# Performance work log

Measured on AMD Instinct MI355X. Metric: run time of the kernel, lower is better.

## Reference

```python
import jax, jax.numpy as jnp
import numpy as np

N, E, D = 50000, 800000, 128
NODE_IN, EDGE_IN, STEPS = 19, 4, 5
EPS = 1e-5

def leaky(x):
    return jnp.where(x > 0, x, 0.05 * x)

def mlp3(x, W1, b1, W2, b2, W3, b3):
    x = leaky(x @ W1 + b1)
    x = leaky(x @ W2 + b2)
    return x @ W3 + b3

def layer_norm(x, g, b):
    m = jnp.mean(x, axis=-1, keepdims=True)
    v = jnp.var(x, axis=-1, keepdims=True)
    return (x - m) * jax.lax.rsqrt(v + EPS) * g + b

def batch_norm(x, g, b):
    # training-mode BatchNorm1d: biased batch stats over node dim
    m = jnp.mean(x, axis=0)
    v = jnp.var(x, axis=0)
    return (x - m) * jax.lax.rsqrt(v + EPS) * g + b

def gcn_conv(x, src, dst, W, b):
    # PyG GCNConv: add self loops, sym-normalize by deg^{-1/2}, aggregate at dst
    h = x @ W  # [N, D]
    deg = jax.ops.segment_sum(jnp.ones(E, x.dtype), dst, num_segments=N) + 1.0
    dis = jax.lax.rsqrt(deg)
    msg = h[src] * (dis[src] * dis[dst])[:, None]  # [E, D]
    agg = jax.ops.segment_sum(msg, dst, num_segments=N) + h * (dis * dis)[:, None]
    return agg + b


def setup_inputs() -> dict:
    key = jax.random.key(0)
    ks = iter(jax.random.split(key, 64))
    w = lambda shape: jax.random.normal(next(ks), shape, jnp.float32) * 0.05
    z = lambda: jnp.zeros((D,), jnp.float32)
    o = lambda: jnp.ones((D,), jnp.float32)
    inp = {
        'node_feat': jax.random.normal(next(ks), (N, NODE_IN), jnp.float32),
        'edge_feat': jax.random.normal(next(ks), (E, EDGE_IN), jnp.float32),
        'edge_index': jax.random.randint(next(ks), (2, E), 0, N, jnp.int32),
        'enc_node_W1': w((NODE_IN, D)), 'enc_node_b1': z(),
        'enc_node_W2': w((D, D)), 'enc_node_b2': z(),
        'enc_node_W3': w((D, D)), 'enc_node_b3': z(),
        'enc_node_ln_g': o(), 'enc_node_ln_b': z(),
        'enc_edge_W1': w((EDGE_IN, D)), 'enc_edge_b1': z(),
        'enc_edge_W2': w((D, D)), 'enc_edge_b2': z(),
        'enc_edge_W3': w((D, D)), 'enc_edge_b3': z(),
        'enc_edge_ln_g': o(), 'enc_edge_ln_b': z(),
        'proc_W': w((STEPS, 2, D, D)),
        'proc_b': jnp.zeros((STEPS, 2, D), jnp.float32),
        'proc_bn_g': jnp.ones((STEPS, D), jnp.float32),
        'proc_bn_b': jnp.zeros((STEPS, D), jnp.float32),
        'dec_W1': w((D, D)), 'dec_b1': z(),
        'dec_W2': w((D, D)), 'dec_b2': z(),
        'dec_W3': w((D, D)), 'dec_b3': z(),
        'dec_ln_g': o(), 'dec_ln_b': z(),
    }
    return inp


def reference(node_feat, edge_feat, edge_index,
              enc_node_W1, enc_node_b1, enc_node_W2, enc_node_b2, enc_node_W3, enc_node_b3,
              enc_node_ln_g, enc_node_ln_b,
              enc_edge_W1, enc_edge_b1, enc_edge_W2, enc_edge_b2, enc_edge_W3, enc_edge_b3,
              enc_edge_ln_g, enc_edge_ln_b,
              proc_W, proc_b, proc_bn_g, proc_bn_b,
              dec_W1, dec_b1, dec_W2, dec_b2, dec_W3, dec_b3, dec_ln_g, dec_ln_b):
    src, dst = edge_index[0], edge_index[1]
    # encode
    hn = layer_norm(mlp3(node_feat, enc_node_W1, enc_node_b1, enc_node_W2, enc_node_b2,
                         enc_node_W3, enc_node_b3), enc_node_ln_g, enc_node_ln_b)
    he = layer_norm(mlp3(edge_feat, enc_edge_W1, enc_edge_b1, enc_edge_W2, enc_edge_b2,
                         enc_edge_W3, enc_edge_b3), enc_edge_ln_g, enc_edge_ln_b)
    # scatter-mean edge features onto source nodes
    cnt = jax.ops.segment_sum(jnp.ones(E, hn.dtype), src, num_segments=N)
    hn = hn + jax.ops.segment_sum(he, src, num_segments=N) / jnp.maximum(cnt, 1.0)[:, None]
    # 5 residual GCN processor steps (GCNConv -> LeakyReLU -> BN -> GCNConv)
    for s in range(STEPS):
        x = gcn_conv(hn, src, dst, proc_W[s, 0], proc_b[s, 0])
        x = batch_norm(leaky(x), proc_bn_g[s], proc_bn_b[s])
        x = gcn_conv(x, src, dst, proc_W[s, 1], proc_b[s, 1])
        hn = hn + x
    # decode
    return layer_norm(mlp3(hn, dec_W1, dec_b1, dec_W2, dec_b2, dec_W3, dec_b3),
                      dec_ln_g, dec_ln_b)
```

## Files before the change

### kernel.cpp

```cpp
#include <hip/hip_runtime.h>

#define NN 50000
#define NE 800000
#define DD 128
#define LN_EPS 1e-5f

typedef __attribute__((ext_vector_type(8))) short v8s;
typedef __attribute__((ext_vector_type(4))) unsigned v4u;
typedef __attribute__((ext_vector_type(4))) float f32x4;
typedef __attribute__((ext_vector_type(2))) float f32x2;

union CvtHL { v4u u; v8s s; };

__device__ __forceinline__ float leakyf(float x){ return x > 0.f ? x : 0.05f*x; }
__device__ __forceinline__ short f2bf(float f){
  unsigned u = __float_as_uint(f);
  u = (u + 0x7fffu + ((u >> 16) & 1u)) >> 16;
  return (short)u;
}
__device__ __forceinline__ float bf2f(unsigned short h){
  return __uint_as_float(((unsigned)h) << 16);
}
__device__ __forceinline__ unsigned cvt_pk_bf16(float a, float b){
  unsigned r;
  asm("v_cvt_pk_bf16_f32 %0, %1, %2" : "=v"(r) : "v"(a), "v"(b));
  return r;
}
__device__ __forceinline__ f32x2 pk_add(f32x2 a, f32x2 b){
  f32x2 r; asm("v_pk_add_f32 %0, %1, %2" : "=v"(r) : "v"(a), "v"(b)); return r;
}
__device__ __forceinline__ f32x2 pk_mul(f32x2 a, f32x2 b){
  f32x2 r; asm("v_pk_mul_f32 %0, %1, %2" : "=v"(r) : "v"(a), "v"(b)); return r;
}
__device__ __forceinline__ unsigned pack_hi16(unsigned u0, unsigned u1){
  return __builtin_amdgcn_perm(u1, u0, 0x07060302u);
}
__device__ __forceinline__ short2 f2bf2v(float v){
  unsigned u = __float_as_uint(v);
  short hi = (short)(u >> 16);
  float lo = v - __uint_as_float(u & 0xffff0000u);
  return make_short2(hi, f2bf(lo));
}

__global__ void pack_small_kernel(const float* __restrict__ nW1,
                                  short* __restrict__ nWh, short* __restrict__ nWl,
                                  const float* __restrict__ eW1, const float* __restrict__ eb1,
                                  short* __restrict__ eWp)
{
  int idx = blockIdx.x*256 + threadIdx.x;
  int k = idx >> 7, n = idx & 127;
  size_t o = ((size_t)(k >> 3)*128 + n)*8 + (k & 7);
  if (blockIdx.y == 0) {
    float v = (k < 19) ? nW1[k*128 + n] : 0.f;
    short2 t = f2bf2v(v);
    nWh[o] = t.x; nWl[o] = t.y;
  } else {
    short v = 0;
    if (k < 4)        v = f2bf2v(eW1[k*128 + n]).x;
    else if (k < 8)   v = f2bf2v(eW1[(k-4)*128 + n]).y;
    else if (k < 12)  v = f2bf2v(eW1[(k-8)*128 + n]).x;
    else if (k == 12) v = f2bf2v(eb1[n]).x;
    else if (k == 13) v = f2bf2v(eb1[n]).y;
    eWp[o] = v;
  }
}

#define NPACK 12
struct PackArgs { const float* src[NPACK]; short* dh[NPACK]; short* dl[NPACK]; };

__global__ void pack_many_kernel(PackArgs pa)
{
  int m = blockIdx.y;
  int idx = blockIdx.x*256 + threadIdx.x;
  int k = idx >> 7, n = idx & 127;
  float v = pa.src[m][k*128 + n];
  short2 t = f2bf2v(v);
  size_t o = ((size_t)(k >> 3)*128 + n)*8 + (k & 7);
  pa.dh[m][o] = t.x; pa.dl[m][o] = t.y;
}

#define MFMA3(ah, al, bh, bl, ac) \
  ac = __builtin_amdgcn_mfma_f32_16x16x32_bf16(al, bh, ac, 0,0,0); \
  ac = __builtin_amdgcn_mfma_f32_16x16x32_bf16(ah, bl, ac, 0,0,0); \
  ac = __builtin_amdgcn_mfma_f32_16x16x32_bf16(ah, bh, ac, 0,0,0);

#define MFMA2(ah, bh, bl, ac) \
  ac = __builtin_amdgcn_mfma_f32_16x16x32_bf16(ah, bl, ac, 0,0,0); \
  ac = __builtin_amdgcn_mfma_f32_16x16x32_bf16(ah, bh, ac, 0,0,0);

#define SPLIT8(f0, f1, h, l) { \
  unsigned u0=__float_as_uint(f0.x), u1=__float_as_uint(f0.y), u2=__float_as_uint(f0.z), u3=__float_as_uint(f0.w); \
  unsigned u4=__float_as_uint(f1.x), u5=__float_as_uint(f1.y), u6=__float_as_uint(f1.z), u7=__float_as_uint(f1.w); \
  CvtHL ch_, cl_; \
  ch_.u = (v4u){ pack_hi16(u0,u1), pack_hi16(u2,u3), pack_hi16(u4,u5), pack_hi16(u6,u7) }; \
  cl_.u = (v4u){ \
    cvt_pk_bf16(f0.x-__uint_as_float(u0&0xffff0000u), f0.y-__uint_as_float(u1&0xffff0000u)), \
    cvt_pk_bf16(f0.z-__uint_as_float(u2&0xffff0000u), f0.w-__uint_as_float(u3&0xffff0000u)), \
    cvt_pk_bf16(f1.x-__uint_as_float(u4&0xffff0000u), f1.y-__uint_as_float(u5&0xffff0000u)), \
    cvt_pk_bf16(f1.z-__uint_as_float(u6&0xffff0000u), f1.w-__uint_as_float(u7&0xffff0000u)) }; \
  h = ch_.s; l = cl_.s; }

#define EPI_PK(accv, bv2, DOBIAS, p01, p23) { \
  f32x2 x01 = (f32x2){(accv)[0], (accv)[1]}; \
  f32x2 x23 = (f32x2){(accv)[2], (accv)[3]}; \
  if (DOBIAS) { x01 = pk_add(x01, bv2); x23 = pk_add(x23, bv2); } \
  f32x2 m01 = pk_mul(x01, (f32x2)(0.05f)); \
  f32x2 m23 = pk_mul(x23, (f32x2)(0.05f)); \
  p01 = cvt_pk_bf16(fmaxf(x01.x, m01.x), fmaxf(x01.y, m01.y)); \
  p23 = cvt_pk_bf16(fmaxf(x23.x, m23.x), fmaxf(x23.y, m23.y)); }

template<int IN_W, bool SCATTER>
__global__ __launch_bounds__(256)
void mlp_mfma_kernel(const float* __restrict__ x, int nrows,
                     const short* __restrict__ W1h, const short* __restrict__ W1l,
                     const float* __restrict__ b1,
                     const short* __restrict__ W2h, const short* __restrict__ W2l,
                     const float* __restrict__ b2,
                     const short* __restrict__ W3h, const short* __restrict__ W3l,
                     const float* __restrict__ b3,
                     const float* __restrict__ g, const float* __restrict__ bb,
                     float* __restrict__ out,
                     const int* __restrict__ sidx,
                     const int* __restrict__ eperm,
                     const float* __restrict__ invcnt)
{
  constexpr int L1K = (IN_W + 31) / 32;
  constexpr bool EDGE1 = (SCATTER && IN_W == 4);
  __shared__ __align__(16) short Hh[128*136];
  __shared__ float lnS[128][2], lnQ[128][2];
  __shared__ int sidx_s[128];
  __shared__ __align__(16) uint4 xstage[SCATTER ? 128 : 1];

  const int tid  = threadIdx.x;
  const int lane = tid & 63, wave = tid >> 6;
  const int wr = wave >> 1, wc = wave & 1;
  const int quad = lane >> 4, low = lane & 15;
  const int row0 = blockIdx.x * 128;

  if (SCATTER) {
    if (tid < 128) {
      int e = eperm[row0 + tid];
      float4 f = ((const float4*)x)[e];
      unsigned u0=__float_as_uint(f.x), u1=__float_as_uint(f.y);
      unsigned u2=__float_as_uint(f.z), u3=__float_as_uint(f.w);
      uint4 st;
      st.x = pack_hi16(u0,u1);
      st.y = pack_hi16(u2,u3);
      st.z = cvt_pk_bf16(f.x-__uint_as_float(u0&0xffff0000u), f.y-__uint_as_float(u1&0xffff0000u));
      st.w = cvt_pk_bf16(f.z-__uint_as_float(u2&0xffff0000u), f.w-__uint_as_float(u3&0xffff0000u));
      xstage[tid] = st;
      sidx_s[tid] = sidx[row0 + tid];
    }
    __syncthreads();
  }

  f32x4 acc[4][4];

  #pragma unroll
  for (int tm=0;tm<4;tm++)
    #pragma unroll
    for (int tn=0;tn<4;tn++) acc[tm][tn] = (f32x4)0.f;

  if constexpr (EDGE1) {
    v8s ah[4], bh[4];
    #pragma unroll
    for (int tm=0;tm<4;tm++) {
      int lr = wr*64 + tm*16 + low;
      v8s h = (v8s)0;
      if (quad == 0) {
        uint4 st = xstage[lr];
        CvtHL c_; c_.u = (v4u){ st.x, st.y, st.x, st.y };
        h = c_.s;
      } else if (quad == 1) {
        uint4 st = xstage[lr];
        CvtHL c_; c_.u = (v4u){ st.z, st.w, 0x3F803F80u, 0u };
        h = c_.s;
      }
      ah[tm] = h;
    }
    #pragma unroll
    for (int tn=0;tn<4;tn++) {
      size_t o = ((size_t)quad*128 + wc*64 + tn*16 + low)*8;
      bh[tn] = *(const v8s*)(W1h + o);
    }
    #pragma unroll
    for (int tm=0;tm<4;tm++)
      #pragma unroll
      for (int tn=0;tn<4;tn++)
        acc[tm][tn] = __builtin_amdgcn_mfma_f32_16x16x32_bf16(ah[tm], bh[tn], acc[tm][tn], 0,0,0);
  } else {
    for (int ks = 0; ks < L1K; ks++) {
      v8s ah[4], al[4], bh[4], bl[4];
      #pragma unroll
      for (int tm=0;tm<4;tm++) {
        int lr = wr*64 + tm*16 + low;
        v8s h = (v8s)0, l = (v8s)0;
        if (IN_W % 32 == 0) {
          int r = row0 + lr;
          if (r < nrows) {
            const float* p = x + (size_t)r*IN_W + ks*32 + quad*8;
            float4 f0 = *(const float4*)p;
            float4 f1 = *(const float4*)(p + 4);
            SPLIT8(f0, f1, h, l);
          }
        } else {
          int r = row0 + lr;
          #pragma unroll
          for (int j=0;j<8;j++) {
            int k = ks*32 + quad*8 + j;
            if (k < IN_W && r < nrows) {
              short2 t = f2bf2v(x[(size_t)r*IN_W + k]);
              h[j] = t.x; l[j] = t.y;
            }
          }
        }
        ah[tm] = h; al[tm] = l;
      }
      #pragma unroll
      for (int tn=0;tn<4;tn++) {
        size_t o = ((size_t)(ks*4+quad)*128 + wc*64 + tn*16 + low)*8;
        bh[tn] = *(const v8s*)(W1h + o);
        bl[tn] = *(const v8s*)(W1l + o);
      }
      #pragma unroll
      for (int tm=0;tm<4;tm++)
        #pragma unroll
        for (int tn=0;tn<4;tn++) { MFMA3(ah[tm], al[tm], bh[tn], bl[tn], acc[tm][tn]); }
    }
  }
  #pragma unroll
  for (int tn=0;tn<4;tn++) {
    float bv = EDGE1 ? 0.f : b1[wc*64 + tn*16 + low];
    f32x2 bv2 = (f32x2)(bv);
    #pragma unroll
    for (int tm=0;tm<4;tm++) {
      unsigned p01, p23;
      EPI_PK(acc[tm][tn], bv2, !EDGE1, p01, p23);
      int base = (wr*64+tm*16+quad*4)*136 + wc*64+tn*16+low;
      Hh[base]     = (short)p01;
      Hh[base+136] = (short)(p01>>16);
      Hh[base+272] = (short)p23;
      Hh[base+408] = (short)(p23>>16);
    }
  }
  __syncthreads();

  #pragma unroll
  for (int tm=0;tm<4;tm++)
    #pragma unroll
    for (int tn=0;tn<4;tn++) acc[tm][tn] = (f32x4)0.f;
  #pragma unroll
  for (int ks=0;ks<4;ks++) {
    v8s ah[4], bh[4], bl[4];
    #pragma unroll
    for (int tm=0;tm<4;tm++)
      ah[tm] = *(const v8s*)&Hh[(wr*64+tm*16+low)*136 + ks*32 + quad*8];
    #pragma unroll
    for (int tn=0;tn<4;tn++) {
      size_t o = ((size_t)(ks*4+quad)*128 + wc*64 + tn*16 + low)*8;
      bh[tn] = *(const v8s*)(W2h + o);
      bl[tn] = *(const v8s*)(W2l + o);
    }
    #pragma unroll
    for (int tm=0;tm<4;tm++)
      #pragma unroll
      for (int tn=0;tn<4;tn++) { MFMA2(ah[tm], bh[tn], bl[tn], acc[tm][tn]); }
  }
  __syncthreads();
  #pragma unroll
  for (int tn=0;tn<4;tn++) {
    float bv = b2[wc*64 + tn*16 + low];
    f32x2 bv2 = (f32x2)(bv);
    #pragma unroll
    for (int tm=0;tm<4;tm++) {
      unsigned p01, p23;
      EPI_PK(acc[tm][tn], bv2, true, p01, p23);
      int base = (wr*64+tm*16+quad*4)*136 + wc*64+tn*16+low;
      Hh[base]     = (short)p01;
      Hh[base+136] = (short)(p01>>16);
      Hh[base+272] = (short)p23;
      Hh[base+408] = (short)(p23>>16);
    }
  }
  __syncthreads();

  #pragma unroll
  for (int tm=0;tm<4;tm++)
    #pragma unroll
    for (int tn=0;tn<4;tn++) acc[tm][tn] = (f32x4)0.f;
  #pragma unroll
  for (int ks=0;ks<4;ks++) {
    v8s ah[4], bh[4], bl[4];
    #pragma unroll
    for (int tm=0;tm<4;tm++)
      ah[tm] = *(const v8s*)&Hh[(wr*64+tm*16+low)*136 + ks*32 + quad*8];
    #pragma unroll
    for (int tn=0;tn<4;tn++) {
      size_t o = ((size_t)(ks*4+quad)*128 + wc*64 + tn*16 + low)*8;
      bh[tn] = *(const v8s*)(W3h + o);
      bl[tn] = *(const v8s*)(W3l + o);
    }
    #pragma unroll
    for (int tm=0;tm<4;tm++)
      #pragma unroll
      for (int tn=0;tn<4;tn++) { MFMA2(ah[tm], bh[tn], bl[tn], acc[tm][tn]); }
  }
  #pragma unroll
  for (int tn=0;tn<4;tn++) {
    float bv = b3[wc*64 + tn*16 + low];
    #pragma unroll
    for (int tm=0;tm<4;tm++)
      #pragma unroll
      for (int i=0;i<4;i++) acc[tm][tn][i] += bv;
  }

  {
    float ct[16];
    #pragma unroll
    for (int tm=0;tm<4;tm++)
      #pragma unroll
      for (int i=0;i<4;i++)
        ct[tm*4+i] = acc[tm][0][i] + acc[tm][1][i] + acc[tm][2][i] + acc[tm][3][i];
    #pragma unroll
    for (int st=0; st<4; st++) {
      const int mm = 1 << st;
      const bool hbit = ((low >> st) & 1) != 0;
      #pragma unroll
      for (int p=0; p < (16>>st); p+=2) {
        float snd = hbit ? ct[p]   : ct[p+1];
        float kp  = hbit ? ct[p+1] : ct[p];
        ct[p>>1] = kp + __shfl_xor(snd, mm);
      }
    }
    { int r = wr*64 + (low>>2)*16 + quad*4 + (low&3); lnS[r][wc] = ct[0]; }
    #pragma unroll
    for (int tm=0;tm<4;tm++)
      #pragma unroll
      for (int i=0;i<4;i++)
        ct[tm*4+i] = acc[tm][0][i]*acc[tm][0][i] + acc[tm][1][i]*acc[tm][1][i]
                   + acc[tm][2][i]*acc[tm][2][i] + acc[tm][3][i]*acc[tm][3][i];
    #pragma unroll
    for (int st=0; st<4; st++) {
      const int mm = 1 << st;
      const bool hbit = ((low >> st) & 1) != 0;
      #pragma unroll
      for (int p=0; p < (16>>st); p+=2) {
        float snd = hbit ? ct[p]   : ct[p+1];
        float kp  = hbit ? ct[p+1] : ct[p];
        ct[p>>1] = kp + __shfl_xor(snd, mm);
      }
    }
    { int r = wr*64 + (low>>2)*16 + quad*4 + (low&3); lnQ[r][wc] = ct[0]; }
  }
  __syncthreads();

  float g4[4], bb4[4];
  #pragma unroll
  for (int tn=0;tn<4;tn++) { int c = wc*64+tn*16+low; g4[tn] = g[c]; bb4[tn] = bb[c]; }

  #pragma unroll
  for (int tm=0;tm<4;tm++)
    #pragma unroll
    for (int i=0;i<4;i++) {
      int r = wr*64 + tm*16 + quad*4 + i;
      float2 S2 = *(const float2*)&lnS[r][0];
      float2 Q2 = *(const float2*)&lnQ[r][0];
      float s = S2.x + S2.y;
      float q = Q2.x + Q2.y;
      float m = s * (1.f/128.f);
      float var = q * (1.f/128.f) - m*m;
      float rs = rsqrtf(var + LN_EPS);
      int gr = row0 + r;
      if (!SCATTER && gr >= nrows) continue;
      float v0 = (acc[tm][0][i] - m) * rs * g4[0] + bb4[0];
      float v1 = (acc[tm][1][i] - m) * rs * g4[1] + bb4[1];
      float v2 = (acc[tm][2][i] - m) * rs * g4[2] + bb4[2];
      float v3 = (acc[tm][3][i] - m) * rs * g4[3] + bb4[3];
      if (SCATTER) {
        unsigned p01 = cvt_pk_bf16(v0, v1), p23 = cvt_pk_bf16(v2, v3);
        int base = r*132 + wc*64 + low;
        Hh[base]    = (short)p01;
        Hh[base+16] = (short)(p01>>16);
        Hh[base+32] = (short)p23;
        Hh[base+48] = (short)(p23>>16);
      } else {
        size_t ob = (size_t)gr*DD + wc*64 + low;
        out[ob]    = v0;
        out[ob+16] = v1;
        out[ob+32] = v2;
        out[ob+48] = v3;
      }
    }

  if (SCATTER) {
    __syncthreads();
    const unsigned* H32 = (const unsigned*)Hh;
    int cp = tid & 63;
    int gI = tid >> 6;
    int rbeg = gI*32, rend = rbeg + 32;
    unsigned pv = H32[rbeg*66 + cp];
    float a0 = __uint_as_float(pv << 16), a1 = __uint_as_float(pv & 0xffff0000u);
    int cur = __builtin_amdgcn_readfirstlane(sidx_s[rbeg]);
    for (int r = rbeg + 1; r < rend; r++) {
      int sv = __builtin_amdgcn_readfirstlane(sidx_s[r]);
      unsigned hv = H32[r*66 + cp];
      if (sv != cur) {
        float ic = invcnt[cur];
        atomicAdd(&out[(size_t)cur*DD + 2*cp],     a0*ic);
        atomicAdd(&out[(size_t)cur*DD + 2*cp + 1], a1*ic);
        a0 = __uint_as_float(hv << 16); a1 = __uint_as_float(hv & 0xffff0000u);
        cur = sv;
      } else {
        a0 += __uint_as_float(hv << 16); a1 += __uint_as_float(hv & 0xffff0000u);
      }
    }
    float ic = invcnt[cur];
    atomicAdd(&out[(size_t)cur*DD + 2*cp],     a0*ic);
    atomicAdd(&out[(size_t)cur*DD + 2*cp + 1], a1*ic);
  }
}

__global__ __launch_bounds__(256)
void gemm_mfma_kernel(const float* __restrict__ x,
                      const short* __restrict__ Wh, const short* __restrict__ Wl,
                      const float* __restrict__ initv, const float* __restrict__ rowscale,
                      unsigned short* __restrict__ outbf, int nrows)
{
  const int tid  = threadIdx.x;
  const int lane = tid & 63, wave = tid >> 6;
  const int wr = wave >> 1, wc = wave & 1;
  const int quad = lane >> 4, low = lane & 15;
  const int row0 = blockIdx.x * 64;

  f32x4 acc[2][4];
  #pragma unroll
  for (int tm=0;tm<2;tm++)
    #pragma unroll
    for (int tn=0;tn<4;tn++) acc[tm][tn] = (f32x4)0.f;

  #pragma unroll
  for (int ks=0;ks<4;ks++) {
    v8s ah[2], al[2], bh[4], bl[4];
    #pragma unroll
    for (int tm=0;tm<2;tm++) {
      int r = row0 + wr*32 + tm*16 + low;
      v8s h = (v8s)0, l = (v8s)0;
      if (r < nrows) {
        const float* p = x + (size_t)r*DD + ks*32 + quad*8;
        float4 f0 = *(const float4*)p;
        float4 f1 = *(const float4*)(p + 4);
        SPLIT8(f0, f1, h, l);
      }
      ah[tm] = h; al[tm] = l;
    }
    #pragma unroll
    for (int tn=0;tn<4;tn++) {
      size_t o = ((size_t)(ks*4+quad)*128 + wc*64 + tn*16 + low)*8;
      bh[tn] = *(const v8s*)(Wh + o);
      bl[tn] = *(const v8s*)(Wl + o);
    }
    #pragma unroll
    for (int tm=0;tm<2;tm++)
      #pragma unroll
      for (int tn=0;tn<4;tn++) { MFMA3(ah[tm], al[tm], bh[tn], bl[tn], acc[tm][tn]); }
  }

  float iv4[4];
  #pragma unroll
  for (int tn=0;tn<4;tn++) iv4[tn] = initv ? initv[wc*64 + tn*16 + low] : 0.f;

  #pragma unroll
  for (int tm=0;tm<2;tm++)
    #pragma unroll
    for (int i=0;i<4;i++) {
      int gr = row0 + wr*32 + tm*16 + quad*4 + i;
      if (gr >= nrows) continue;
      float sc = rowscale ? rowscale[gr] : 1.f;
      float v0 = (acc[tm][0][i] + iv4[0]) * sc;
      float v1 = (acc[tm][1][i] + iv4[1]) * sc;
      float v2 = (acc[tm][2][i] + iv4[2]) * sc;
      float v3 = (acc[tm][3][i] + iv4[3]) * sc;
      unsigned p01 = cvt_pk_bf16(v0, v1), p23 = cvt_pk_bf16(v2, v3);
      size_t base = (size_t)gr*DD + wc*64 + low;
      outbf[base]    = (unsigned short)p01;
      outbf[base+16] = (unsigned short)(p01>>16);
      outbf[base+32] = (unsigned short)p23;
      outbf[base+48] = (unsigned short)(p23>>16);
    }
}

__global__ __launch_bounds__(256)
void gemm_bf_mfma_kernel(const unsigned short* __restrict__ xb,
                         const short* __restrict__ Wh, const short* __restrict__ Wl,
                         const float* __restrict__ initv, const float* __restrict__ rowscale,
                         unsigned short* __restrict__ outbf, int nrows)
{
  const int tid  = threadIdx.x;
  const int lane = tid & 63, wave = tid >> 6;
  const int wr = wave >> 1, wc = wave & 1;
  const int quad = lane >> 4, low = lane & 15;
  const int row0 = blockIdx.x * 64;

  f32x4 acc[2][4];
  #pragma unroll
  for (int tm=0;tm<2;tm++)
    #pragma unroll
    for (int tn=0;tn<4;tn++) acc[tm][tn] = (f32x4)0.f;

  #pragma unroll
  for (int ks=0;ks<4;ks++) {
    v8s ah[2], bh[4], bl[4];
    #pragma unroll
    for (int tm=0;tm<2;tm++) {
      int r = row0 + wr*32 + tm*16 + low;
      ah[tm] = (r < nrows) ? *(const v8s*)(xb + (size_t)r*DD + ks*32 + quad*8) : (v8s)0;
    }
    #pragma unroll
    for (int tn=0;tn<4;tn++) {
      size_t o = ((size_t)(ks*4+quad)*128 + wc*64 + tn*16 + low)*8;
      bh[tn] = *(const v8s*)(Wh + o);
      bl[tn] = *(const v8s*)(Wl + o);
    }
    #pragma unroll
    for (int tm=0;tm<2;tm++)
      #pragma unroll
      for (int tn=0;tn<4;tn++) { MFMA2(ah[tm], bh[tn], bl[tn], acc[tm][tn]); }
  }

  float iv4[4];
  #pragma unroll
  for (int tn=0;tn<4;tn++) iv4[tn] = initv ? initv[wc*64 + tn*16 + low] : 0.f;

  #pragma unroll
  for (int tm=0;tm<2;tm++)
    #pragma unroll
    for (int i=0;i<4;i++) {
      int gr = row0 + wr*32 + tm*16 + quad*4 + i;
      if (gr >= nrows) continue;
      float sc = rowscale ? rowscale[gr] : 1.f;
      float v0 = (acc[tm][0][i] + iv4[0]) * sc;
      float v1 = (acc[tm][1][i] + iv4[1]) * sc;
      float v2 = (acc[tm][2][i] + iv4[2]) * sc;
      float v3 = (acc[tm][3][i] + iv4[3]) * sc;
      unsigned p01 = cvt_pk_bf16(v0, v1), p23 = cvt_pk_bf16(v2, v3);
      size_t base = (size_t)gr*DD + wc*64 + low;
      outbf[base]    = (unsigned short)p01;
      outbf[base+16] = (unsigned short)(p01>>16);
      outbf[base+32] = (unsigned short)p23;
      outbf[base+48] = (unsigned short)(p23>>16);
    }
}

__global__ __launch_bounds__(256)
void gcn_agg_kernel(const unsigned* __restrict__ hb, const int* __restrict__ rowptr,
                    const int* __restrict__ csr_src, const float* __restrict__ dis,
                    const float* __restrict__ bias, const float* __restrict__ resid,
                    float* __restrict__ outf, unsigned* __restrict__ outb, int mode)
{
  const int wv = __builtin_amdgcn_readfirstlane(threadIdx.x >> 6);
  const int lane = threadIdx.x & 63;
  const int i = blockIdx.x*4 + wv;
  if (i >= NN) return;
  unsigned hv = hb[(size_t)i*64 + lane];
  float ax = bf2f((unsigned short)(hv & 0xffff)), ay = bf2f((unsigned short)(hv >> 16));
  const int beg = rowptr[i], end = rowptr[i+1];
  int j = beg;
  for (; j + 16 <= end; j += 16) {
    unsigned v[16];
    #pragma unroll
    for (int k=0;k<16;k++) v[k] = hb[(size_t)csr_src[j+k]*64 + lane];
    #pragma unroll
    for (int k=0;k<16;k++) {
      ax += bf2f((unsigned short)(v[k] & 0xffff));
      ay += bf2f((unsigned short)(v[k] >> 16));
    }
  }
  for (; j + 4 <= end; j += 4) {
    unsigned v[4];
    #pragma unroll
    for (int k=0;k<4;k++) v[k] = hb[(size_t)csr_src[j+k]*64 + lane];
    #pragma unroll
    for (int k=0;k<4;k++) {
      ax += bf2f((unsigned short)(v[k] & 0xffff));
      ay += bf2f((unsigned short)(v[k] >> 16));
    }
  }
  for (; j < end; j++) {
    unsigned v = hb[(size_t)csr_src[j]*64 + lane];
    ax += bf2f((unsigned short)(v & 0xffff));
    ay += bf2f((unsigned short)(v >> 16));
  }
  float di = dis[i];
  float2 bv = ((const float2*)bias)[lane];
  ax = ax*di + bv.x; ay = ay*di + bv.y;
  size_t o = (size_t)i*64 + lane;
  if (mode == 0) {
    outb[o] = cvt_pk_bf16(leakyf(ax), leakyf(ay));
  } else {
    float2 rs = ((const float2*)resid)[o];
    float2 r; r.x = rs.x + ax; r.y = rs.y + ay;
    ((float2*)outf)[o] = r;
  }
}

__global__ void count_kernel(const int* __restrict__ src, const int* __restrict__ dst,
                             int* __restrict__ cnt_src, int* __restrict__ deg_dst)
{
  int e = blockIdx.x*blockDim.x + threadIdx.x;
  if (e < NE) {
    atomicAdd(&cnt_src[src[e]], 1);
    atomicAdd(&deg_dst[dst[e]], 1);
  }
}

__global__ void scan2_kernel(const int* __restrict__ a0, int* __restrict__ r0, int* __restrict__ n0,
                             float* __restrict__ aux0,
                             const int* __restrict__ a1, int* __restrict__ r1, int* __restrict__ n1,
                             float* __restrict__ aux1)
{
  const int* a = blockIdx.x ? a1 : a0;
  int* r = blockIdx.x ? r1 : r0;
  int* n = blockIdx.x ? n1 : n0;
  float* aux = blockIdx.x ? aux1 : aux0;
  const int T = 256;
  int tid = threadIdx.x;
  int chunk = (NN + T - 1) / T;
  int begin = tid*chunk, end = begin + chunk; if (end > NN) end = NN; if (begin > NN) begin = NN;
  int s = 0;
  for (int i = begin; i < end; i++) s += a[i];
  __shared__ int ps[T];
  ps[tid] = s; __syncthreads();
  for (int off = 1; off < T; off <<= 1) {
    int v = 0;
    if (tid >= off) v = ps[tid - off];
    __syncthreads();
    if (tid >= off) ps[tid] += v;
    __syncthreads();
  }
  int base = (tid == 0) ? 0 : ps[tid-1];
  for (int i = begin; i < end; i++) {
    r[i] = base; n[i] = base; base += a[i];
    aux[i] = blockIdx.x ? (1.0f / fmaxf((float)a[i], 1.0f)) : rsqrtf((float)a[i] + 1.0f);
  }
  if (tid == T-1) r[NN] = base;
}

__global__ void fill_both_kernel(const int* __restrict__ src, const int* __restrict__ dst,
                                 int* __restrict__ nextp, int* __restrict__ csr_src,
                                 int* __restrict__ nexts, int* __restrict__ eperm,
                                 int* __restrict__ srcsorted)
{
  int e = blockIdx.x*blockDim.x + threadIdx.x;
  if (e < NE) {
    int s = src[e];
    int pos = atomicAdd(&nextp[dst[e]], 1);
    csr_src[pos] = s;
    int ps = atomicAdd(&nexts[s], 1);
    eperm[ps] = e;
    srcsorted[ps] = s;
  }
}

__global__ __launch_bounds__(256)
void bn_stats_kernel(const unsigned* __restrict__ yb32, float* __restrict__ sums)
{
  int cp  = threadIdx.x & 63;
  int grp = threadIdx.x >> 6;
  float s0=0.f, s1=0.f, q0=0.f, q1=0.f;
  for (int i = blockIdx.x*4 + grp; i < NN; i += gridDim.x*4) {
    unsigned v = yb32[(size_t)i*64 + cp];
    float a = __uint_as_float(v << 16);
    float b = __uint_as_float(v & 0xffff0000u);
    s0 += a; q0 += a*a; s1 += b; q1 += b*b;
  }
  __shared__ float red[256][4];
  red[threadIdx.x][0]=s0; red[threadIdx.x][1]=s1; red[threadIdx.x][2]=q0; red[threadIdx.x][3]=q1;
  __syncthreads();
  if (grp == 0) {
    float t0=0.f,t1=0.f,t2=0.f,t3=0.f;
    #pragma unroll
    for (int g2=0; g2<4; g2++) {
      t0+=red[g2*64+cp][0]; t1+=red[g2*64+cp][1]; t2+=red[g2*64+cp][2]; t3+=red[g2*64+cp][3];
    }
    atomicAdd(&sums[2*cp],      t0);
    atomicAdd(&sums[2*cp+1],    t1);
    atomicAdd(&sums[DD+2*cp],   t2);
    atomicAdd(&sums[DD+2*cp+1], t3);
  }
}

__global__ __launch_bounds__(256)
void bn_fold_kernel(const float* __restrict__ sums, const float* __restrict__ g,
                    const float* __restrict__ b, const float* __restrict__ W2,
                    short* __restrict__ Wfh, short* __restrict__ Wfl,
                    float* __restrict__ cvec)
{
  __shared__ float scale_s[DD], shift_s[DD];
  int tid = threadIdx.x;
  if (tid < DD) {
    float m = sums[tid] / (float)NN;
    float var = sums[DD + tid] / (float)NN - m*m;
    float is = rsqrtf(var + LN_EPS);
    float sc = is * g[tid];
    scale_s[tid] = sc;
    shift_s[tid] = b[tid] - m * sc;
  }
  __syncthreads();
  int col = tid & 127, kh = tid >> 7;
  float cpart = 0.f;
  #pragma unroll
  for (int kk = 0; kk < 4; kk++) {
    int k = blockIdx.x*8 + kh*4 + kk;
    float w = W2[k*DD + col];
    short2 t = f2bf2v(w * scale_s[k]);
    size_t o = ((size_t)(k >> 3)*128 + col)*8 + (k & 7);
    Wfh[o] = t.x; Wfl[o] = t.y;
    cpart += shift_s[k] * w;
  }
  atomicAdd(&cvec[col], cpart);
}

extern "C" void kernel_launch(void* const* d_in, const int* in_sizes, int n_in,
                              void* d_out, int out_size, void* d_ws, size_t ws_size,
                              hipStream_t stream)
{
  const float* node_feat = (const float*)d_in[0];
  const float* edge_feat = (const float*)d_in[1];
  const int*   edge_index = (const int*)d_in[2];
  const int* src = edge_index;
  const int* dst = edge_index + NE;

  const float* enW1 = (const float*)d_in[3];  const float* enb1 = (const float*)d_in[4];
  const float* enW2 = (const float*)d_in[5];  const float* enb2 = (const float*)d_in[6];
  const float* enW3 = (const float*)d_in[7];  const float* enb3 = (const float*)d_in[8];
  const float* enlg = (const float*)d_in[9];  const float* enlb = (const float*)d_in[10];

  const float* eeW1 = (const float*)d_in[11]; const float* eeb1 = (const float*)d_in[12];
  const float* eeW2 = (const float*)d_in[13]; const float* eeb2 = (const float*)d_in[14];
  const float* eeW3 = (const float*)d_in[15]; const float* eeb3 = (const float*)d_in[16];
  const float* eelg = (const float*)d_in[17]; const float* eelb = (const float*)d_in[18];

  const float* procW = (const float*)d_in[19];
  const float* procB = (const float*)d_in[20];
  const float* bnG   = (const float*)d_in[21];
  const float* bnB   = (const float*)d_in[22];

  const float* dW1 = (const float*)d_in[23]; const float* db1 = (const float*)d_in[24];
  const float* dW2 = (const float*)d_in[25]; const float* db2 = (const float*)d_in[26];
  const float* dW3 = (const float*)d_in[27]; const float* db3 = (const float*)d_in[28];
  const float* dlg = (const float*)d_in[29]; const float* dlb = (const float*)d_in[30];

  char* ws = (char*)d_ws;
  size_t off = 0;
  auto alloc = [&](size_t bytes) -> void* {
    void* p = ws + off;
    off = (off + bytes + 255) & ~(size_t)255;
    return p;
  };
  float* hn     = (float*)alloc((size_t)NN*DD*4);
  unsigned short* hbf = (unsigned short*)alloc((size_t)NN*DD*2);
  unsigned short* ybf = (unsigned short*)alloc((size_t)NN*DD*2);
  float* dis    = (float*)alloc(NN*4);
  float* invcnt = (float*)alloc(NN*4);
  float* bnsums5 = (float*)alloc(5*3*DD*4);
  int* deg    = (int*)alloc(NN*4);
  int* cnt    = (int*)alloc(NN*4);
  int* rowptr = (int*)alloc((NN+1)*4);
  int* nextp  = (int*)alloc(NN*4);
  int* srow   = (int*)alloc((NN+1)*4);
  int* nexts  = (int*)alloc(NN*4);
  int* csr    = (int*)alloc((size_t)NE*4);
  int* eperm  = (int*)alloc((size_t)NE*4);
  int* srcsorted = (int*)alloc((size_t)NE*4);
  auto allocW = [&](int kp) { return (short*)alloc((size_t)kp*128*2); };
  short *pN1h=allocW(32),  *pN1l=allocW(32);
  short *pN2h=allocW(128), *pN2l=allocW(128);
  short *pN3h=allocW(128), *pN3l=allocW(128);
  short *pE1h=allocW(32),  *pE1l=allocW(32);
  short *pE2h=allocW(128), *pE2l=allocW(128);
  short *pE3h=allocW(128), *pE3l=allocW(128);
  short *pD1h=allocW(128), *pD1l=allocW(128);
  short *pD2h=allocW(128), *pD2l=allocW(128);
  short *pD3h=allocW(128), *pD3l=allocW(128);
  short *pP0h[5], *pP0l[5];
  for (int s = 0; s < 5; s++) { pP0h[s]=allocW(128); pP0l[s]=allocW(128); }
  short *pWfh=allocW(128), *pWfl=allocW(128);

  (void)hipMemsetAsync(deg, 0, NN*4, stream);
  (void)hipMemsetAsync(cnt, 0, NN*4, stream);
  (void)hipMemsetAsync(bnsums5, 0, 5*3*DD*4, stream);

  PackArgs pa;
  const float* s128[NPACK] = { enW2, enW3, eeW2, eeW3, dW1, dW2, dW3,
                               procW + 0*(size_t)DD*DD*2, procW + 1*(size_t)DD*DD*2,
                               procW + 2*(size_t)DD*DD*2, procW + 3*(size_t)DD*DD*2,
                               procW + 4*(size_t)DD*DD*2 };
  short* d128h[NPACK] = { pN2h, pN3h, pE2h, pE3h, pD1h, pD2h, pD3h,
                          pP0h[0], pP0h[1], pP0h[2], pP0h[3], pP0h[4] };
  short* d128l[NPACK] = { pN2l, pN3l, pE2l, pE3l, pD1l, pD2l, pD3l,
                          pP0l[0], pP0l[1], pP0l[2], pP0l[3], pP0l[4] };
  for (int m = 0; m < NPACK; m++) { pa.src[m]=s128[m]; pa.dh[m]=d128h[m]; pa.dl[m]=d128l[m]; }
  pack_many_kernel<<<dim3(64, NPACK), 256, 0, stream>>>(pa);
  pack_small_kernel<<<dim3(16, 2), 256, 0, stream>>>(enW1, pN1h, pN1l, eeW1, eeb1, pE1h);

  count_kernel<<<(NE+255)/256, 256, 0, stream>>>(src, dst, cnt, deg);
  scan2_kernel<<<2, 256, 0, stream>>>(deg, rowptr, nextp, dis, cnt, srow, nexts, invcnt);
  fill_both_kernel<<<(NE+255)/256, 256, 0, stream>>>(src, dst, nextp, csr, nexts, eperm, srcsorted);

  const int GN  = (NN + 127) / 128;
  const int GE  = NE / 128;
  const int GG  = (NN + 63) / 64;
  const int GA  = (NN + 3) / 4;

  mlp_mfma_kernel<19, false><<<GN, 256, 0, stream>>>(node_feat, NN,
      pN1h, pN1l, enb1, pN2h, pN2l, enb2, pN3h, pN3l, enb3, enlg, enlb, hn,
      nullptr, nullptr, nullptr);
  mlp_mfma_kernel<4, true><<<GE, 256, 0, stream>>>(edge_feat, NE,
      pE1h, pE1l, eeb1, pE2h, pE2l, eeb2, pE3h, pE3l, eeb3, eelg, eelb, hn,
      srcsorted, eperm, invcnt);

  for (int s = 0; s < 5; s++) {
    const float* Wc2 = procW + (size_t)(s*2+1)*DD*DD;
    const float* b0  = procB + (size_t)(s*2+0)*DD;
    const float* b1p = procB + (size_t)(s*2+1)*DD;
    float* sums = bnsums5 + (size_t)s*3*DD;
    float* cvec = sums + 2*DD;

    gemm_mfma_kernel<<<GG, 256, 0, stream>>>(hn, pP0h[s], pP0l[s], nullptr, dis, hbf, NN);
    gcn_agg_kernel<<<GA, 256, 0, stream>>>((const unsigned*)hbf, rowptr, csr, dis,
                                           b0, nullptr, nullptr, (unsigned*)ybf, 0);
    bn_stats_kernel<<<512, 256, 0, stream>>>((const unsigned*)ybf, sums);
    bn_fold_kernel<<<16, 256, 0, stream>>>(sums, bnG + s*DD, bnB + s*DD, Wc2, pWfh, pWfl, cvec);
    gemm_bf_mfma_kernel<<<GG, 256, 0, stream>>>(ybf, pWfh, pWfl, cvec, dis, hbf, NN);
    gcn_agg_kernel<<<GA, 256, 0, stream>>>((const unsigned*)hbf, rowptr, csr, dis,
                                           b1p, hn, hn, nullptr, 1);
  }

  mlp_mfma_kernel<128, false><<<GN, 256, 0, stream>>>(hn, NN,
      pD1h, pD1l, db1, pD2h, pD2l, db2, pD3h, pD3l, db3, dlg, dlb, (float*)d_out,
      nullptr, nullptr, nullptr);
}
```

Before: 1.346 ms.

## Split GCN aggregation across feature slices with 4 nodes per wavefront

The aggregation kernel now assigns each wavefront four destination nodes, with 16 lanes per node covering a 64-byte slice of the feature row. A second grid dimension of 4 spreads the 128 features across four blocks. This gives more independent neighbor-walk chains per wavefront to hide gather latency and balances uneven degrees across lanes. The cost is that each block re-reads rowptr/csr indices and every gather is only 64 bytes wide. It also depends on NN being divisible by 16, because the bounds check was removed.

```diff
diff --git a/kernel.cpp b/kernel.cpp
--- a/kernel.cpp
+++ b/kernel.cpp
@@ -557,20 +557,24 @@
                     const float* __restrict__ bias, const float* __restrict__ resid,
                     float* __restrict__ outf, unsigned* __restrict__ outb, int mode)
 {
-  const int wv = __builtin_amdgcn_readfirstlane(threadIdx.x >> 6);
   const int lane = threadIdx.x & 63;
-  const int i = blockIdx.x*4 + wv;
-  if (i >= NN) return;
-  unsigned hv = hb[(size_t)i*64 + lane];
-  float ax = bf2f((unsigned short)(hv & 0xffff)), ay = bf2f((unsigned short)(hv >> 16));
-  const int beg = rowptr[i], end = rowptr[i+1];
+  const int wv   = threadIdx.x >> 6;
+  const int q    = lane >> 4;
+  const int c    = lane & 15;
+  const int soff = blockIdx.y * 16 + c;
+  const int i    = blockIdx.x * 16 + wv * 4 + q;
+
+  unsigned hv = hb[(size_t)i * 64 + soff];
+  float ax = bf2f((unsigned short)(hv & 0xffff));
+  float ay = bf2f((unsigned short)(hv >> 16));
+  const int beg = rowptr[i], end = rowptr[i + 1];
   int j = beg;
   for (; j + 16 <= end; j += 16) {
     unsigned v[16];
     #pragma unroll
-    for (int k=0;k<16;k++) v[k] = hb[(size_t)csr_src[j+k]*64 + lane];
-    #pragma unroll
-    for (int k=0;k<16;k++) {
+    for (int k = 0; k < 16; k++) v[k] = hb[(size_t)csr_src[j + k] * 64 + soff];
+    #pragma unroll
+    for (int k = 0; k < 16; k++) {
       ax += bf2f((unsigned short)(v[k] & 0xffff));
       ay += bf2f((unsigned short)(v[k] >> 16));
     }
@@ -578,22 +582,22 @@
   for (; j + 4 <= end; j += 4) {
     unsigned v[4];
     #pragma unroll
-    for (int k=0;k<4;k++) v[k] = hb[(size_t)csr_src[j+k]*64 + lane];
-    #pragma unroll
-    for (int k=0;k<4;k++) {
+    for (int k = 0; k < 4; k++) v[k] = hb[(size_t)csr_src[j + k] * 64 + soff];
+    #pragma unroll
+    for (int k = 0; k < 4; k++) {
       ax += bf2f((unsigned short)(v[k] & 0xffff));
       ay += bf2f((unsigned short)(v[k] >> 16));
     }
   }
   for (; j < end; j++) {
-    unsigned v = hb[(size_t)csr_src[j]*64 + lane];
+    unsigned v = hb[(size_t)csr_src[j] * 64 + soff];
     ax += bf2f((unsigned short)(v & 0xffff));
     ay += bf2f((unsigned short)(v >> 16));
   }
   float di = dis[i];
-  float2 bv = ((const float2*)bias)[lane];
-  ax = ax*di + bv.x; ay = ay*di + bv.y;
-  size_t o = (size_t)i*64 + lane;
+  float2 bv = ((const float2*)bias)[soff];
+  ax = ax * di + bv.x; ay = ay * di + bv.y;
+  size_t o = (size_t)i * 64 + soff;
   if (mode == 0) {
     outb[o] = cvt_pk_bf16(leakyf(ax), leakyf(ay));
   } else {
@@ -810,7 +814,7 @@
   const int GN  = (NN + 127) / 128;
   const int GE  = NE / 128;
   const int GG  = (NN + 63) / 64;
-  const int GA  = (NN + 3) / 4;
+  const dim3 GAS(NN/16, 4);
 
   mlp_mfma_kernel<19, false><<<GN, 256, 0, stream>>>(node_feat, NN,
       pN1h, pN1l, enb1, pN2h, pN2l, enb2, pN3h, pN3l, enb3, enlg, enlb, hn,
@@ -827,13 +831,13 @@
     float* cvec = sums + 2*DD;
 
     gemm_mfma_kernel<<<GG, 256, 0, stream>>>(hn, pP0h[s], pP0l[s], nullptr, dis, hbf, NN);
-    gcn_agg_kernel<<<GA, 256, 0, stream>>>((const unsigned*)hbf, rowptr, csr, dis,
-                                           b0, nullptr, nullptr, (unsigned*)ybf, 0);
+    gcn_agg_kernel<<<GAS, 256, 0, stream>>>((const unsigned*)hbf, rowptr, csr, dis,
+                                            b0, nullptr, nullptr, (unsigned*)ybf, 0);
     bn_stats_kernel<<<512, 256, 0, stream>>>((const unsigned*)ybf, sums);
     bn_fold_kernel<<<16, 256, 0, stream>>>(sums, bnG + s*DD, bnB + s*DD, Wc2, pWfh, pWfl, cvec);
     gemm_bf_mfma_kernel<<<GG, 256, 0, stream>>>(ybf, pWfh, pWfl, cvec, dis, hbf, NN);
-    gcn_agg_kernel<<<GA, 256, 0, stream>>>((const unsigned*)hbf, rowptr, csr, dis,
-                                           b1p, hn, hn, nullptr, 1);
+    gcn_agg_kernel<<<GAS, 256, 0, stream>>>((const unsigned*)hbf, rowptr, csr, dis,
+                                            b1p, hn, hn, nullptr, 1);
   }
 
   mlp_mfma_kernel<128, false><<<GN, 256, 0, stream>>>(hn, NN,
```

After: 1.520 ms. +13.0%, slower.
